# Optimization experiments

Measured on AMD Instinct MI355X. Metric: run time of the kernel, lower is better.

The kernel has to match this reference:

```python
import jax, jax.numpy as jnp
import numpy as np

B, S, D, H = 2, 2048, 1024, 16
DH = D // H  # 64


def setup_inputs() -> dict:
    key = jax.random.key(0)
    ks = jax.random.split(key, 9)
    def rn(k, shape, scale=1.0):
        return jax.random.normal(k, shape, dtype=jnp.float32) * scale
    w_scale = 1.0 / np.sqrt(D)
    return {
        "queries": rn(ks[0], (B, S, D)),
        "keys": rn(ks[1], (B, S, D)),
        "values": rn(ks[2], (B, S, D)),
        "Wq": rn(ks[3], (D, D), w_scale),
        "bq": rn(ks[4], (D,), w_scale),
        "Wk": rn(ks[5], (D, D), w_scale),
        "bk": rn(ks[6], (D,), w_scale),
        "Wv": rn(ks[7], (D, D), w_scale),
        "bv": rn(ks[8], (D,), w_scale),
    }


def _split_heads(x):
    # torch: cat(split(x, DH, dim=-1), dim=0) -> index (h*B + b); equivalent to
    # [B,S,H,DH] -> [H,B,S,DH]
    bsz, slen, _ = x.shape
    return x.reshape(bsz, slen, H, DH).transpose(2, 0, 1, 3)


def reference(queries, keys, values, Wq, bq, Wk, bk, Wv, bv):
    # Linear projections (W stored so that y = x @ W + b)
    Q = queries @ Wq + bq
    K = keys @ Wk + bk
    V = values @ Wv + bv

    Qh = _split_heads(Q)  # [H,B,S,DH]
    Kh = _split_heads(K)
    Vh = _split_heads(V)

    scale = 1.0 / jnp.sqrt(jnp.asarray(DH, dtype=Qh.dtype))
    scores = jnp.einsum("hbqd,hbkd->hbqk", Qh, Kh) * scale  # [H,B,S,S]
    attn = jax.nn.softmax(scores, axis=-1)  # dropout_rate=0 -> identity
    out = jnp.einsum("hbqk,hbkd->hbqd", attn, Vh)  # [H,B,S,DH]

    # torch: cat(split(out, B, dim=0), dim=2) -> [B,S,H*DH] with head h in slice h
    out = out.transpose(1, 2, 0, 3).reshape(queries.shape[0], queries.shape[1], D)
    return out + queries  # residual; NOTE: W_O is defined but unused in the original forward
```

## Files before the change

### kernel.cpp

```cpp
#include <hip/hip_runtime.h>
#include <hip/hip_bf16.h>
#include <math.h>

#define BB 2
#define SS 2048
#define DD 1024
#define HH 16
#define DHH 64
#define MM (BB * SS)

typedef float f32x4 __attribute__((ext_vector_type(4)));
typedef float f32x16 __attribute__((ext_vector_type(16)));
typedef __bf16 bf16x8 __attribute__((ext_vector_type(8)));
typedef unsigned int u32x2 __attribute__((ext_vector_type(2)));

#define N_QKV ((size_t)MM * DD)
#define N_W   ((size_t)DD * DD)

__device__ unsigned short g_X [3][N_QKV];
__device__ unsigned short g_Q [N_QKV];
__device__ unsigned short g_K [N_QKV];
__device__ unsigned short g_Vt[N_QKV];
__device__ unsigned short g_Wt[3][N_W];

__device__ __forceinline__ unsigned short f2bu(float f) {
    unsigned u = __float_as_uint(f);
    unsigned r = u + 0x7FFFu + ((u >> 16) & 1u);
    return (unsigned short)(r >> 16);
}

union FragU { uint4 u; bf16x8 v; unsigned short s[8]; };
static __device__ __forceinline__ bf16x8 ldfrag(const unsigned short* p) {
    FragU f; f.u = *(const uint4*)p; return f.v;
}

static __device__ __forceinline__ unsigned pkbf(float a, float b) {
    union { __bf16 h[2]; unsigned u; } w;
    w.h[0] = (__bf16)a; w.h[1] = (__bf16)b;
    return w.u;
}

static __device__ __forceinline__ float fexp2(float x) {
#if __has_builtin(__builtin_amdgcn_exp2f)
    return __builtin_amdgcn_exp2f(x);
#else
    float r;
    asm("v_exp_f32 %0, %1" : "=v"(r) : "v"(x));
    return r;
#endif
}

static __device__ __forceinline__ void plswap(unsigned &a, unsigned &b) {
#if __has_builtin(__builtin_amdgcn_permlane32_swap)
    u32x2 r = __builtin_amdgcn_permlane32_swap((int)a, (int)b, false, false);
    a = r[0]; b = r[1];
#else
    asm volatile("v_permlane32_swap_b32 %0, %1" : "+v"(a), "+v"(b));
#endif
}

__global__ __launch_bounds__(256) void prep3(
        const float* __restrict__ x0, const float* __restrict__ x1,
        const float* __restrict__ x2, unsigned short* __restrict__ X,
        const float* __restrict__ W0, const float* __restrict__ W1,
        const float* __restrict__ W2, unsigned short* __restrict__ Wt3)
{
    __shared__ float Ts[64][65];
    const int z = blockIdx.y, t = threadIdx.x;
    if (blockIdx.x < 4096) {
        const float* src = z == 0 ? x0 : (z == 1 ? x1 : x2);
        unsigned short* dst = X + (size_t)z * N_QKV;
        const size_t i = ((size_t)blockIdx.x * 256 + t) * 4;
        const float4 v = *(const float4*)(src + i);
        ushort4 s;
        s.x = f2bu(v.x); s.y = f2bu(v.y); s.z = f2bu(v.z); s.w = f2bu(v.w);
        *(ushort4*)(dst + i) = s;
    } else {
        const float* W = z == 0 ? W0 : (z == 1 ? W1 : W2);
        unsigned short* Wt = Wt3 + (size_t)z * N_W;
        const int bx = blockIdx.x - 4096;
        const int k0 = (bx >> 4) * 64, n0 = (bx & 15) * 64;
#pragma unroll
        for (int i = 0; i < 16; ++i) {
            const int f = t + 256 * i, r = f >> 6, c = f & 63;
            Ts[r][c] = W[(size_t)(k0 + r) * DD + n0 + c];
        }
        __syncthreads();
#pragma unroll
        for (int i = 0; i < 16; ++i) {
            const int f = t + 256 * i, r = f >> 6, c = f & 63;
            Wt[(size_t)(n0 + r) * DD + k0 + c] = f2bu(Ts[c][r]);
        }
    }
}

__global__ __launch_bounds__(256) void proj3(
        const unsigned short* __restrict__ X, const unsigned short* __restrict__ Wt3,
        const float* __restrict__ bq, const float* __restrict__ bk,
        const float* __restrict__ bv,
        unsigned short* __restrict__ Qp, unsigned short* __restrict__ Kp,
        unsigned short* __restrict__ Vtp)
{
    const int bid = blockIdx.x;
    const int xx = bid & 7, j = bid >> 3;
    const int zm = xx * 12 + (j >> 3);
    const int z  = zm >> 5;
    const int m0 = (zm & 31) * 128;
    const int n0 = (j & 7) * 128;

    const unsigned short* xb = X   + (size_t)z * N_QKV;
    const unsigned short* Wt = Wt3 + (size_t)z * N_W;
    const float* bias = z == 0 ? bq : (z == 1 ? bk : bv);
    const float scale = z == 0 ? 0.18033688011112042f : 1.0f;

    __shared__ unsigned short As[128][72];
    __shared__ unsigned short Bs[128][72];
    const int t = threadIdx.x, lane = t & 63, w = t >> 6;
    const int q = lane >> 4, li = lane & 15;
    const int wm = (w >> 1) * 64, wn = (w & 1) * 64;
    const int rs = t >> 3, cs = (t & 7) * 8;

    f32x4 acc[4][4];
#pragma unroll
    for (int mt = 0; mt < 4; ++mt)
#pragma unroll
        for (int nt = 0; nt < 4; ++nt) acc[mt][nt] = (f32x4)0.f;

    uint4 pa0, pa1, pa2, pa3, pb0, pb1, pb2, pb3;
#define PROJ_LD(kk) \
    pa0 = *(const uint4*)(xb + (size_t)(m0 + rs      ) * DD + (kk) + cs); \
    pa1 = *(const uint4*)(xb + (size_t)(m0 + rs + 32 ) * DD + (kk) + cs); \
    pa2 = *(const uint4*)(xb + (size_t)(m0 + rs + 64 ) * DD + (kk) + cs); \
    pa3 = *(const uint4*)(xb + (size_t)(m0 + rs + 96 ) * DD + (kk) + cs); \
    pb0 = *(const uint4*)(Wt + (size_t)(n0 + rs      ) * DD + (kk) + cs); \
    pb1 = *(const uint4*)(Wt + (size_t)(n0 + rs + 32 ) * DD + (kk) + cs); \
    pb2 = *(const uint4*)(Wt + (size_t)(n0 + rs + 64 ) * DD + (kk) + cs); \
    pb3 = *(const uint4*)(Wt + (size_t)(n0 + rs + 96 ) * DD + (kk) + cs);

    PROJ_LD(0)

    for (int kk = 0; kk < DD; kk += 64) {
        *(uint4*)&As[rs     ][cs] = pa0;
        *(uint4*)&As[rs + 32][cs] = pa1;
        *(uint4*)&As[rs + 64][cs] = pa2;
        *(uint4*)&As[rs + 96][cs] = pa3;
        *(uint4*)&Bs[rs     ][cs] = pb0;
        *(uint4*)&Bs[rs + 32][cs] = pb1;
        *(uint4*)&Bs[rs + 64][cs] = pb2;
        *(uint4*)&Bs[rs + 96][cs] = pb3;
        __syncthreads();
        if (kk + 64 < DD) { PROJ_LD(kk + 64) }
#pragma unroll
        for (int ks = 0; ks < 64; ks += 32) {
            bf16x8 a[4], b[4];
#pragma unroll
            for (int mt = 0; mt < 4; ++mt) a[mt] = ldfrag(&As[wm + mt * 16 + li][ks + q * 8]);
#pragma unroll
            for (int nt = 0; nt < 4; ++nt) b[nt] = ldfrag(&Bs[wn + nt * 16 + li][ks + q * 8]);
#pragma unroll
            for (int mt = 0; mt < 4; ++mt)
#pragma unroll
                for (int nt = 0; nt < 4; ++nt)
                    acc[mt][nt] = __builtin_amdgcn_mfma_f32_16x16x32_bf16(
                        a[mt], b[nt], acc[mt][nt], 0, 0, 0);
        }
        __syncthreads();
    }
#undef PROJ_LD

    float bvv[4];
#pragma unroll
    for (int nt = 0; nt < 4; ++nt) bvv[nt] = bias[n0 + wn + nt * 16 + li];

    if (z < 2) {
        unsigned short* out = z == 0 ? Qp : Kp;
#pragma unroll
        for (int mt = 0; mt < 4; ++mt)
#pragma unroll
            for (int nt = 0; nt < 4; ++nt)
#pragma unroll
                for (int reg = 0; reg < 4; ++reg) {
                    const int m = m0 + wm + mt * 16 + q * 4 + reg;
                    out[(size_t)m * DD + n0 + wn + nt * 16 + li] =
                        f2bu((acc[mt][nt][reg] + bvv[nt]) * scale);
                }
    } else {
        const int b = m0 >> 11;
        const int h = (n0 + wn) >> 6;
#pragma unroll
        for (int mt = 0; mt < 4; ++mt)
#pragma unroll
            for (int nt = 0; nt < 4; ++nt) {
                const int s = (m0 & (SS - 1)) + wm + mt * 16 + q * 4;
                const int dh = nt * 16 + li;
                ushort4 sv;
                sv.x = f2bu(acc[mt][nt][0] + bvv[nt]);
                sv.y = f2bu(acc[mt][nt][1] + bvv[nt]);
                sv.z = f2bu(acc[mt][nt][2] + bvv[nt]);
                sv.w = f2bu(acc[mt][nt][3] + bvv[nt]);
                *(ushort4*)(Vtp + ((size_t)((b * HH + h) * DHH + dh)) * SS + s) = sv;
            }
    }
}

__global__ __launch_bounds__(512, 1) void attn11(
        const unsigned short* __restrict__ Qg, const unsigned short* __restrict__ Kg,
        const unsigned short* __restrict__ Vtg,
        const float* __restrict__ queries, float* __restrict__ outp)
{
    __shared__ unsigned short Kb[4][64][64];
    __shared__ unsigned short Vb[4][64][64];
    __shared__ float Lp[8][32];

    const int t = threadIdx.x, lane = t & 63, w = t >> 6;
    const int col = lane & 31;
    const int hi  = lane >> 5;

    const int bid = blockIdx.x;
    const int p  = (bid & 7) * 4 + ((bid >> 3) >> 3);
    const int qt = (bid >> 3) & 7;
    const int h = p & 15, b = p >> 4;

    const int sr = t >> 3;
    const int sc = t & 7;

    const unsigned short* Kbase = Kg  + (size_t)(b * SS) * DD + h * DHH;
    const unsigned short* Vbase = Vtg + ((size_t)((b * HH + h) * DHH)) * SS;

    bf16x8 qa[4];
    {
        const unsigned short* qp =
            Qg + (size_t)(b * SS + qt * 256 + w * 32 + col) * DD + h * DHH + hi * 8;
#pragma unroll
        for (int i = 0; i < 4; ++i) qa[i] = ldfrag(qp + i * 16);
    }

    f32x16 o0 = (f32x16)0.f, o1 = (f32x16)0.f;
    float lsum = 0.f;
    const int xr2 = (col ^ (col >> 3)) & 7;
    const int wsw = (sr ^ (sr >> 3)) & 7;

    uint4 aK0, aV0, aK1, aV1, bK0, bV0, bK1, bV1;
#define LD2(K0, V0, K1, V1, s0) \
    K0 = *(const uint4*)(Kbase + (size_t)((s0)      + sr) * DD + sc * 8); \
    V0 = *(const uint4*)(Vbase + (size_t)sr * SS + (s0)      + sc * 8); \
    K1 = *(const uint4*)(Kbase + (size_t)((s0) + 64 + sr) * DD + sc * 8); \
    V1 = *(const uint4*)(Vbase + (size_t)sr * SS + (s0) + 64 + sc * 8);

#define ST2(K0, V0, K1, V1, b0, b1) \
    *(uint4*)&Kb[b0][sr][(sc ^ wsw) * 8] = K0; \
    *(uint4*)&Vb[b0][sr][(sc ^ wsw) * 8] = V0; \
    *(uint4*)&Kb[b1][sr][(sc ^ wsw) * 8] = K1; \
    *(uint4*)&Vb[b1][sr][(sc ^ wsw) * 8] = V1;

#define TILE(BUF)                                                             \
    {                                                                         \
        f32x16 st0 = (f32x16)0.f, st1 = (f32x16)0.f;                          \
        __builtin_amdgcn_s_setprio(1);                                        \
        _Pragma("unroll")                                                     \
        for (int i = 0; i < 4; ++i) {                                         \
            const int sl = (i * 2 + hi) ^ xr2;                                \
            bf16x8 ka0 = ldfrag(&Kb[BUF][col     ][sl * 8]);                  \
            bf16x8 ka1 = ldfrag(&Kb[BUF][col + 32][(sl ^ 4) * 8]);            \
            st0 = __builtin_amdgcn_mfma_f32_32x32x16_bf16(ka0, qa[i], st0, 0, 0, 0); \
            st1 = __builtin_amdgcn_mfma_f32_32x32x16_bf16(ka1, qa[i], st1, 0, 0, 0); \
        }                                                                     \
        __builtin_amdgcn_s_setprio(0);                                        \
        unsigned pkw[4][4];                                                   \
        float ls = 0.f;                                                       \
        _Pragma("unroll")                                                     \
        for (int s = 0; s < 2; ++s) {                                         \
            float pe[8];                                                      \
            _Pragma("unroll")                                                 \
            for (int r = 0; r < 8; ++r) pe[r] = fexp2(st0[8 * s + r]);        \
            ls += ((pe[0] + pe[1]) + (pe[2] + pe[3])) + ((pe[4] + pe[5]) + (pe[6] + pe[7])); \
            pkw[s][0] = pkbf(pe[0], pe[1]); pkw[s][1] = pkbf(pe[2], pe[3]);   \
            pkw[s][2] = pkbf(pe[4], pe[5]); pkw[s][3] = pkbf(pe[6], pe[7]);   \
        }                                                                     \
        _Pragma("unroll")                                                     \
        for (int s = 0; s < 2; ++s) {                                         \
            float pe[8];                                                      \
            _Pragma("unroll")                                                 \
            for (int r = 0; r < 8; ++r) pe[r] = fexp2(st1[8 * s + r]);        \
            ls += ((pe[0] + pe[1]) + (pe[2] + pe[3])) + ((pe[4] + pe[5]) + (pe[6] + pe[7])); \
            pkw[2 + s][0] = pkbf(pe[0], pe[1]); pkw[2 + s][1] = pkbf(pe[2], pe[3]); \
            pkw[2 + s][2] = pkbf(pe[4], pe[5]); pkw[2 + s][3] = pkbf(pe[6], pe[7]); \
        }                                                                     \
        lsum += ls;                                                           \
        __builtin_amdgcn_s_setprio(1);                                        \
        _Pragma("unroll")                                                     \
        for (int c = 0; c < 4; ++c) {                                         \
            unsigned A0 = pkw[c][0], B0 = pkw[c][2];                          \
            unsigned A1 = pkw[c][1], B1 = pkw[c][3];                          \
            plswap(A0, B0); plswap(A1, B1);                                   \
            FragU pf;                                                         \
            pf.u.x = A0; pf.u.y = A1; pf.u.z = B0; pf.u.w = B1;               \
            const int vl = (c * 2 + hi) ^ xr2;                                \
            bf16x8 vb0 = ldfrag(&Vb[BUF][col     ][vl * 8]);                  \
            bf16x8 vb1 = ldfrag(&Vb[BUF][col + 32][(vl ^ 4) * 8]);            \
            o0 = __builtin_amdgcn_mfma_f32_32x32x16_bf16(pf.v, vb0, o0, 0, 0, 0); \
            o1 = __builtin_amdgcn_mfma_f32_32x32x16_bf16(pf.v, vb1, o1, 0, 0, 0); \
        }                                                                     \
        __builtin_amdgcn_s_setprio(0);                                        \
    }

    LD2(aK0, aV0, aK1, aV1, 0)
    ST2(aK0, aV0, aK1, aV1, 0, 1)
    LD2(bK0, bV0, bK1, bV1, 128)
    __syncthreads();

    for (int tt = 0; tt < SS; tt += 256) {
        if (tt + 256 < SS) { LD2(aK0, aV0, aK1, aV1, tt + 256) }
        TILE(0)
        ST2(bK0, bV0, bK1, bV1, 2, 3)
        TILE(1)
        __syncthreads();
        if (tt + 384 < SS) { LD2(bK0, bV0, bK1, bV1, tt + 384) }
        TILE(2)
        if (tt + 256 < SS) { ST2(aK0, aV0, aK1, aV1, 0, 1) }
        TILE(3)
        if (tt + 256 < SS) __syncthreads();
    }
#undef TILE
#undef LD2
#undef ST2

    const float lt = lsum + __shfl_xor(lsum, 32);
    if (lane < 32) Lp[w][lane] = lt;
    __syncthreads();

    const size_t gbase = (size_t)(b * SS + qt * 256 + w * 32) * DD + h * DHH + col;
#pragma unroll
    for (int reg = 0; reg < 16; ++reg) {
        const int rl = (reg & 3) + 8 * (reg >> 2) + 4 * hi;
        const float li = 1.f / Lp[w][rl];
        const size_t g = gbase + (size_t)rl * DD;
        outp[g]      = o0[reg] * li + queries[g];
        outp[g + 32] = o1[reg] * li + queries[g + 32];
    }
}

extern "C" void kernel_launch(void* const* d_in, const int* in_sizes, int n_in,
                              void* d_out, int out_size, void* d_ws, size_t ws_size,
                              hipStream_t stream) {
    const float* queries = (const float*)d_in[0];
    const float* keys    = (const float*)d_in[1];
    const float* values  = (const float*)d_in[2];
    const float* Wq      = (const float*)d_in[3];
    const float* bq      = (const float*)d_in[4];
    const float* Wk      = (const float*)d_in[5];
    const float* bk      = (const float*)d_in[6];
    const float* Wv      = (const float*)d_in[7];
    const float* bv      = (const float*)d_in[8];
    float* outp = (float*)d_out;

    const size_t need = (6 * N_QKV + 3 * N_W) * sizeof(unsigned short);
    unsigned short *Xp, *Qp, *Kp, *Vtp, *Wtp;
    if (ws_size >= need) {
        Xp  = (unsigned short*)d_ws;
        Qp  = Xp + 3 * N_QKV;
        Kp  = Qp + N_QKV;
        Vtp = Kp + N_QKV;
        Wtp = Vtp + N_QKV;
    } else {
        hipGetSymbolAddress((void**)&Xp,  HIP_SYMBOL(g_X));
        hipGetSymbolAddress((void**)&Qp,  HIP_SYMBOL(g_Q));
        hipGetSymbolAddress((void**)&Kp,  HIP_SYMBOL(g_K));
        hipGetSymbolAddress((void**)&Vtp, HIP_SYMBOL(g_Vt));
        hipGetSymbolAddress((void**)&Wtp, HIP_SYMBOL(g_Wt));
    }

    const dim3 bp(256);
    prep3<<<dim3(4096 + 256, 3), bp, 0, stream>>>(queries, keys, values, Xp,
                                                  Wq, Wk, Wv, Wtp);
    proj3<<<dim3(768), bp, 0, stream>>>(Xp, Wtp, bq, bk, bv, Qp, Kp, Vtp);
    attn11<<<dim3(256), dim3(512), 0, stream>>>(Qp, Kp, Vtp, queries, outp);
}
```

Measured before the change: 193.5 us.

## Load projection GEMM tiles directly into LDS with XOR-swizzled layout

The QKV projection GEMM now uses global_load_lds DMA (16 bytes per lane) to move X and W tiles straight into shared memory, with no staging through registers. The shared tiles lose their padding and use an XOR swizzle on the 8-element slot index, so fragment reads avoid bank conflicts. The goal is to cut VGPR use and the register-to-LDS store instructions. The trade-off is that the next tile's load is now issued only after compute and the trailing barrier on a single buffer. That removes the old overlap of global loads with MFMA work and relies on the load being complete at the next barrier.

```diff
diff --git a/kernel.cpp b/kernel.cpp
--- a/kernel.cpp
+++ b/kernel.cpp
@@ -57,6 +57,12 @@
 #else
     asm volatile("v_permlane32_swap_b32 %0, %1" : "+v"(a), "+v"(b));
 #endif
+}
+
+static __device__ __forceinline__ void gload16(const unsigned short* g, unsigned short* l) {
+    __builtin_amdgcn_global_load_lds(
+        (const __attribute__((address_space(1))) unsigned int*)g,
+        (__attribute__((address_space(3))) unsigned int*)l, 16, 0, 0);
 }
 
 __global__ __launch_bounds__(256) void prep3(
@@ -94,7 +100,7 @@
     }
 }
 
-__global__ __launch_bounds__(256) void proj3(
+__global__ __launch_bounds__(256) void proj4(
         const unsigned short* __restrict__ X, const unsigned short* __restrict__ Wt3,
         const float* __restrict__ bq, const float* __restrict__ bk,
         const float* __restrict__ bv,
@@ -113,12 +119,34 @@
     const float* bias = z == 0 ? bq : (z == 1 ? bk : bv);
     const float scale = z == 0 ? 0.18033688011112042f : 1.0f;
 
-    __shared__ unsigned short As[128][72];
-    __shared__ unsigned short Bs[128][72];
+    __shared__ unsigned short As[128][64];
+    __shared__ unsigned short Bs[128][64];
     const int t = threadIdx.x, lane = t & 63, w = t >> 6;
     const int q = lane >> 4, li = lane & 15;
     const int wm = (w >> 1) * 64, wn = (w & 1) * 64;
-    const int rs = t >> 3, cs = (t & 7) * 8;
+
+    const int lrow = lane >> 3, lslot = lane & 7;
+    const unsigned short* gA[4];
+    const unsigned short* gB[4];
+    unsigned short* lA[4];
+    unsigned short* lB[4];
+#pragma unroll
+    for (int jj = 0; jj < 4; ++jj) {
+        const int r0 = (jj * 4 + w) * 8;
+        const int row = r0 + lrow;
+        const int ss = lslot ^ ((row ^ (row >> 3)) & 7);
+        gA[jj] = xb + (size_t)(m0 + row) * DD + ss * 8;
+        gB[jj] = Wt + (size_t)(n0 + row) * DD + ss * 8;
+        lA[jj] = &As[r0][0];
+        lB[jj] = &Bs[r0][0];
+    }
+
+#define ISSUE(kk) \
+    _Pragma("unroll") \
+    for (int jj = 0; jj < 4; ++jj) { \
+        gload16(gA[jj] + (kk), lA[jj]); \
+        gload16(gB[jj] + (kk), lB[jj]); \
+    }
 
     f32x4 acc[4][4];
 #pragma unroll
@@ -126,37 +154,23 @@
 #pragma unroll
         for (int nt = 0; nt < 4; ++nt) acc[mt][nt] = (f32x4)0.f;
 
-    uint4 pa0, pa1, pa2, pa3, pb0, pb1, pb2, pb3;
-#define PROJ_LD(kk) \
-    pa0 = *(const uint4*)(xb + (size_t)(m0 + rs      ) * DD + (kk) + cs); \
-    pa1 = *(const uint4*)(xb + (size_t)(m0 + rs + 32 ) * DD + (kk) + cs); \
-    pa2 = *(const uint4*)(xb + (size_t)(m0 + rs + 64 ) * DD + (kk) + cs); \
-    pa3 = *(const uint4*)(xb + (size_t)(m0 + rs + 96 ) * DD + (kk) + cs); \
-    pb0 = *(const uint4*)(Wt + (size_t)(n0 + rs      ) * DD + (kk) + cs); \
-    pb1 = *(const uint4*)(Wt + (size_t)(n0 + rs + 32 ) * DD + (kk) + cs); \
-    pb2 = *(const uint4*)(Wt + (size_t)(n0 + rs + 64 ) * DD + (kk) + cs); \
-    pb3 = *(const uint4*)(Wt + (size_t)(n0 + rs + 96 ) * DD + (kk) + cs);
-
-    PROJ_LD(0)
+    ISSUE(0)
 
     for (int kk = 0; kk < DD; kk += 64) {
-        *(uint4*)&As[rs     ][cs] = pa0;
-        *(uint4*)&As[rs + 32][cs] = pa1;
-        *(uint4*)&As[rs + 64][cs] = pa2;
-        *(uint4*)&As[rs + 96][cs] = pa3;
-        *(uint4*)&Bs[rs     ][cs] = pb0;
-        *(uint4*)&Bs[rs + 32][cs] = pb1;
-        *(uint4*)&Bs[rs + 64][cs] = pb2;
-        *(uint4*)&Bs[rs + 96][cs] = pb3;
         __syncthreads();
-        if (kk + 64 < DD) { PROJ_LD(kk + 64) }
-#pragma unroll
-        for (int ks = 0; ks < 64; ks += 32) {
+#pragma unroll
+        for (int ks8 = 0; ks8 < 8; ks8 += 4) {
             bf16x8 a[4], b[4];
 #pragma unroll
-            for (int mt = 0; mt < 4; ++mt) a[mt] = ldfrag(&As[wm + mt * 16 + li][ks + q * 8]);
-#pragma unroll
-            for (int nt = 0; nt < 4; ++nt) b[nt] = ldfrag(&Bs[wn + nt * 16 + li][ks + q * 8]);
+            for (int mt = 0; mt < 4; ++mt) {
+                const int row = wm + mt * 16 + li;
+                a[mt] = ldfrag(&As[row][((q + ks8) ^ ((row ^ (row >> 3)) & 7)) * 8]);
+            }
+#pragma unroll
+            for (int nt = 0; nt < 4; ++nt) {
+                const int row = wn + nt * 16 + li;
+                b[nt] = ldfrag(&Bs[row][((q + ks8) ^ ((row ^ (row >> 3)) & 7)) * 8]);
+            }
 #pragma unroll
             for (int mt = 0; mt < 4; ++mt)
 #pragma unroll
@@ -165,8 +179,9 @@
                         a[mt], b[nt], acc[mt][nt], 0, 0, 0);
         }
         __syncthreads();
-    }
-#undef PROJ_LD
+        if (kk + 64 < DD) { ISSUE(kk + 64) }
+    }
+#undef ISSUE
 
     float bvv[4];
 #pragma unroll
@@ -373,6 +388,6 @@
     const dim3 bp(256);
     prep3<<<dim3(4096 + 256, 3), bp, 0, stream>>>(queries, keys, values, Xp,
                                                   Wq, Wk, Wv, Wtp);
-    proj3<<<dim3(768), bp, 0, stream>>>(Xp, Wtp, bq, bk, bv, Qp, Kp, Vtp);
+    proj4<<<dim3(768), bp, 0, stream>>>(Xp, Wtp, bq, bk, bv, Qp, Kp, Vtp);
     attn11<<<dim3(256), dim3(512), 0, stream>>>(Qp, Kp, Vtp, queries, outp);
 }
```

Result: no change. 195.2 us (+0.9%).
